# Optimization experiments

Hardware: AMD Instinct MI355X
Metric: run time of the kernel (lower is better)

## Reference

```python
import jax, jax.numpy as jnp
import numpy as np
from functools import partial


def conv2d(x, w, b, pad):
    # x: [B,C,H,W], w: [O,I,kh,kw]
    out = jax.lax.conv_general_dilated(
        x, w, window_strides=(1, 1), padding=[(pad, pad), (pad, pad)],
        dimension_numbers=("NCHW", "OIHW", "NCHW"))
    return out + b[None, :, None, None]


def maxpool3x3_s1(x):
    return jax.lax.reduce_window(
        x, -jnp.inf, jax.lax.max, (1, 1, 3, 3), (1, 1, 1, 1),
        padding=((0, 0), (0, 0), (1, 1), (1, 1)))


def bilinear_sample(img, y, x):
    # img: [B,C,H,W]; y, x: [B,H,W] float sample coords. Zero outside bounds.
    def one(im, yy, xx):  # im [C,H,W]
        H, W = im.shape[1], im.shape[2]
        y0 = jnp.floor(yy)
        x0 = jnp.floor(xx)
        wy = yy - y0
        wx = xx - x0
        y0i = y0.astype(jnp.int32)
        x0i = x0.astype(jnp.int32)

        def g(yi, xi):
            valid = (yi >= 0) & (yi < H) & (xi >= 0) & (xi < W)
            yc = jnp.clip(yi, 0, H - 1)
            xc = jnp.clip(xi, 0, W - 1)
            return im[:, yc, xc] * valid[None].astype(im.dtype)

        return (g(y0i, x0i) * ((1 - wy) * (1 - wx))[None]
                + g(y0i, x0i + 1) * ((1 - wy) * wx)[None]
                + g(y0i + 1, x0i) * (wy * (1 - wx))[None]
                + g(y0i + 1, x0i + 1) * (wy * wx)[None])

    return jax.vmap(one)(img, y, x)


def deform_conv2d(x, offset, weight, bias, k, pad):
    # torchvision-style: offset [B, 2*k*k, H, W], pairs are (dy, dx) in
    # row-major kernel order. stride=1, dilation=1.
    B, C, H, W = x.shape
    off = offset.reshape(B, k * k, 2, H, W)
    hh = jnp.arange(H, dtype=x.dtype)[None, :, None]  # [1,H,1]
    ww = jnp.arange(W, dtype=x.dtype)[None, None, :]  # [1,1,W]
    out = jnp.zeros((B, weight.shape[0], H, W), x.dtype)
    for t in range(k * k):
        i, j = t // k, t % k
        y = hh + (i - pad) + off[:, t, 0]  # [B,H,W]
        xc = ww + (j - pad) + off[:, t, 1]
        s = bilinear_sample(x, y, xc)      # [B,C,H,W]
        out = out + jnp.einsum("bchw,oc->bohw", s, weight[:, :, i, j])
    return out + bias[None, :, None, None]


def _mk(key, shape, scale=0.05):
    return jax.random.normal(key, shape, dtype=jnp.float32) * scale


def setup_inputs() -> dict:
    key = jax.random.key(0)
    ks = jax.random.split(key, 20)
    C = 512
    Cb = C // 4  # 128
    B, H, W = 8, 64, 64
    return {
        "x": jax.random.normal(ks[0], (B, C, H, W), dtype=jnp.float32),
        "w_b1": _mk(ks[1], (Cb, C, 1, 1)), "b_b1": jnp.zeros((Cb,), jnp.float32),
        "w_b21": _mk(ks[2], (Cb, C, 1, 1)), "b_b21": jnp.zeros((Cb,), jnp.float32),
        "w_off2": _mk(ks[3], (18, Cb, 3, 3), 0.01), "b_off2": jnp.zeros((18,), jnp.float32),
        "w_ddc2": _mk(ks[4], (Cb, Cb, 3, 3)), "b_ddc2": jnp.zeros((Cb,), jnp.float32),
        "w_b31": _mk(ks[5], (Cb, C, 1, 1)), "b_b31": jnp.zeros((Cb,), jnp.float32),
        "w_off3": _mk(ks[6], (50, Cb, 5, 5), 0.01), "b_off3": jnp.zeros((50,), jnp.float32),
        "w_ddc3": _mk(ks[7], (Cb, Cb, 5, 5)), "b_ddc3": jnp.zeros((Cb,), jnp.float32),
        "w_b4": _mk(ks[8], (Cb, C, 1, 1)), "b_b4": jnp.zeros((Cb,), jnp.float32),
        "w_cc": _mk(ks[9], (C, Cb * 4, 1, 1)), "b_cc": jnp.zeros((C,), jnp.float32),
    }


def reference(x, w_b1, b_b1, w_b21, b_b21, w_off2, b_off2, w_ddc2, b_ddc2,
              w_b31, b_b31, w_off3, b_off3, w_ddc3, b_ddc3, w_b4, b_b4,
              w_cc, b_cc):
    b1 = conv2d(x, w_b1, b_b1, 0)

    b2i = conv2d(x, w_b21, b_b21, 0)
    off2 = conv2d(b2i, w_off2, b_off2, 1)
    b2 = deform_conv2d(b2i, off2, w_ddc2, b_ddc2, k=3, pad=1)

    b3i = conv2d(x, w_b31, b_b31, 0)
    off3 = conv2d(b3i, w_off3, b_off3, 2)
    b3 = deform_conv2d(b3i, off3, w_ddc3, b_ddc3, k=5, pad=2)

    b4 = conv2d(maxpool3x3_s1(x), w_b4, b_b4, 0)

    cat = jnp.concatenate([b1, b2, b3, b4], axis=1) * x
    fused = conv2d(cat, w_cc, b_cc, 0)
    return x + jax.nn.sigmoid(fused)
```

## Files before the change

### kernel.cpp

```cpp
#include <hip/hip_runtime.h>
#include <math.h>

#define HW 4096
typedef short short8 __attribute__((ext_vector_type(8)));
typedef float floatx4 __attribute__((ext_vector_type(4)));

#define O_XBT   0ull
#define O_PXB   33554432ull
#define O_CATB  67108864ull
#define O_WPB   100663296ull
#define O_W4B   101056512ull
#define O_WCCB  101187584ull
#define O_WD2T  101711872ull
#define O_WD3T  102006784ull
#define O_WO2T  102825984ull
#define O_WO3T  102973440ull
#define O_T2B   33554432ull
#define O_T3B   41943040ull
#define O_OFF2  50331648ull
#define O_OFF3  52690944ull

__device__ __forceinline__ unsigned short f2b(float f) {
    union { float f; unsigned u; } v; v.f = f;
    unsigned r = v.u + 0x7FFFu + ((v.u >> 16) & 1u);
    return (unsigned short)(r >> 16);
}
__device__ __forceinline__ float lou(unsigned u) {
    union { unsigned u; float f; } v; v.u = u << 16; return v.f;
}
__device__ __forceinline__ float hiu(unsigned u) {
    union { unsigned u; float f; } v; v.u = u & 0xFFFF0000u; return v.f;
}
__device__ __forceinline__ unsigned pk2(float lo, float hi) {
    return (unsigned)f2b(lo) | ((unsigned)f2b(hi) << 16);
}

__global__ __launch_bounds__(256) void k_prepw(
        const float* __restrict__ w1, const float* __restrict__ w21,
        const float* __restrict__ w31, const float* __restrict__ w4,
        const float* __restrict__ wcc, const float* __restrict__ wd2,
        const float* __restrict__ wd3, const float* __restrict__ wo2,
        const float* __restrict__ wo3, unsigned short* __restrict__ ws8) {
    unsigned i = blockIdx.x * 256 + threadIdx.x;
    unsigned short* wpb  = ws8 + (O_WPB  >> 1);
    unsigned short* w4b  = ws8 + (O_W4B  >> 1);
    unsigned short* wccb = ws8 + (O_WCCB >> 1);
    unsigned short* wd2t = ws8 + (O_WD2T >> 1);
    unsigned short* wd3t = ws8 + (O_WD3T >> 1);
    unsigned short* wo2t = ws8 + (O_WO2T >> 1);
    unsigned short* wo3t = ws8 + (O_WO3T >> 1);
    if (i < 196608) {
        int o = i >> 9;
        float v = (o < 128) ? w1[i] : (o < 256) ? w21[i - 65536] : w31[i - 131072];
        wpb[i] = f2b(v);
    } else if (i < 262144) {
        unsigned j = i - 196608; w4b[j] = f2b(w4[j]);
    } else if (i < 524288) {
        unsigned j = i - 262144; wccb[j] = f2b(wcc[j]);
    } else if (i < 671744) {
        unsigned j = i - 524288; int t = j >> 14, o = (j >> 7) & 127, c = j & 127;
        wd2t[j] = f2b(wd2[((o * 128 + c) * 9) + t]);
    } else if (i < 1081344) {
        unsigned j = i - 671744; int t = j >> 14, o = (j >> 7) & 127, c = j & 127;
        wd3t[j] = f2b(wd3[((o * 128 + c) * 25) + t]);
    } else if (i < 1155072) {
        unsigned j = i - 1081344; int t = j >> 13, o = (j >> 7) & 63, c = j & 127;
        wo2t[j] = (o < 18) ? f2b(wo2[((o * 128 + c) * 9) + t]) : 0;
    } else if (i < 1359872) {
        unsigned j = i - 1155072; int t = j >> 13, o = (j >> 7) & 63, c = j & 127;
        wo3t[j] = (o < 50) ? f2b(wo3[((o * 128 + c) * 25) + t]) : 0;
    }
}

__global__ __launch_bounds__(256) void k_xpose(const float* __restrict__ X,
                                               unsigned short* __restrict__ xbT) {
    __shared__ unsigned short t[32][33];
    const int p0 = blockIdx.x * 32, c0 = blockIdx.y * 32, b = blockIdx.z;
    const int tid = threadIdx.x;
    #pragma unroll
    for (int s = 0; s < 4; ++s) {
        int cl = s * 8 + (tid >> 5), pl = tid & 31;
        t[cl][pl] = f2b(X[((size_t)b * 512 + c0 + cl) * HW + p0 + pl]);
    }
    __syncthreads();
    #pragma unroll
    for (int s = 0; s < 4; ++s) {
        int pl = s * 8 + (tid >> 5), cl = tid & 31;
        xbT[((size_t)b * HW + p0 + pl) * 512 + c0 + cl] = t[cl][pl];
    }
}

__global__ __launch_bounds__(256) void k_pool(const unsigned short* __restrict__ xbT,
                                              unsigned short* __restrict__ pxb) {
    unsigned gid = blockIdx.x * 256 + threadIdx.x;
    int b = gid >> 18;
    unsigned rem = gid & 262143;
    int pos = rem >> 6;
    int cg = (rem & 63) * 8;
    int h = pos >> 6, w = pos & 63;
    const unsigned short* img = xbT + (size_t)b * HW * 512;
    float m[8] = {-INFINITY, -INFINITY, -INFINITY, -INFINITY,
                  -INFINITY, -INFINITY, -INFINITY, -INFINITY};
    #pragma unroll
    for (int dy = -1; dy <= 1; ++dy) {
        int hh = h + dy;
        if (hh < 0 || hh >= 64) continue;
        #pragma unroll
        for (int dx = -1; dx <= 1; ++dx) {
            int ww = w + dx;
            if (ww < 0 || ww >= 64) continue;
            uint4 v = *(const uint4*)(img + ((size_t)(hh * 64 + ww)) * 512 + cg);
            unsigned uu[4] = {v.x, v.y, v.z, v.w};
            #pragma unroll
            for (int e = 0; e < 4; ++e) {
                m[2 * e]     = fmaxf(m[2 * e],     lou(uu[e]));
                m[2 * e + 1] = fmaxf(m[2 * e + 1], hiu(uu[e]));
            }
        }
    }
    uint4 o;
    o.x = pk2(m[0], m[1]); o.y = pk2(m[2], m[3]);
    o.z = pk2(m[4], m[5]); o.w = pk2(m[6], m[7]);
    *(uint4*)(pxb + ((size_t)b * HW + pos) * 512 + cg) = o;
}

#define SA(r,c) SM[(r)*40 + (c)]
#define SB(r,c) SM[5120 + (r)*40 + (c)]
#define SC(r,c) SM[(r)*136 + (c)]
__global__ __launch_bounds__(256) void k_gemm(
        const unsigned short* __restrict__ A, const float* __restrict__ bias,
        const unsigned short* __restrict__ Bm,
        unsigned short* __restrict__ dst, int dStride, int dOff) {
    __shared__ unsigned short SM[17408];
    const int tid = threadIdx.x;
    const int n0 = blockIdx.x * 128;
    const int b = blockIdx.z;
    const int wave = tid >> 6, lane = tid & 63, quad = lane >> 4, lr = lane & 15;
    const int m0w = (wave & 1) * 64, n0w = (wave >> 1) * 64;
    const int srow = tid >> 1, skh = (tid & 1) * 16;
    floatx4 acc[4][4] = {};

    for (int k0 = 0; k0 < 512; k0 += 32) {
        const unsigned short* ga = A + (size_t)srow * 512 + k0 + skh;
        uint4 a0 = *(const uint4*)(ga);
        uint4 a1 = *(const uint4*)(ga + 8);
        const unsigned short* gb = Bm + ((size_t)b * HW + n0 + srow) * 512 + k0 + skh;
        uint4 b0 = *(const uint4*)(gb);
        uint4 b1 = *(const uint4*)(gb + 8);
        __syncthreads();
        *(uint4*)&SA(srow, skh) = a0;
        *(uint4*)&SA(srow, skh + 8) = a1;
        *(uint4*)&SB(srow, skh) = b0;
        *(uint4*)&SB(srow, skh + 8) = b1;
        __syncthreads();
        short8 af[4], bf[4];
        #pragma unroll
        for (int i = 0; i < 4; ++i) af[i] = *(short8*)&SA(m0w + i * 16 + lr, quad * 8);
        #pragma unroll
        for (int j = 0; j < 4; ++j) bf[j] = *(short8*)&SB(n0w + j * 16 + lr, quad * 8);
        #pragma unroll
        for (int i = 0; i < 4; ++i)
            #pragma unroll
            for (int j = 0; j < 4; ++j)
                acc[i][j] = __builtin_amdgcn_mfma_f32_16x16x32_bf16(af[i], bf[j], acc[i][j], 0, 0, 0);
    }
    __syncthreads();
    #pragma unroll
    for (int i = 0; i < 4; ++i) {
        float4 bs = *(const float4*)&bias[m0w + i * 16 + quad * 4];
        #pragma unroll
        for (int j = 0; j < 4; ++j) {
            floatx4 v = acc[i][j];
            int pos = n0w + j * 16 + lr;
            int ch = m0w + i * 16 + quad * 4;
            uint2 st;
            st.x = pk2(v[0] + bs.x, v[1] + bs.y);
            st.y = pk2(v[2] + bs.z, v[3] + bs.w);
            *(uint2*)&SC(pos, ch) = st;
        }
    }
    __syncthreads();
    #pragma unroll
    for (int r = 0; r < 8; ++r) {
        int pos = (tid >> 4) + r * 16;
        *(uint4*)&dst[((size_t)b * HW + n0 + pos) * dStride + dOff + (tid & 15) * 8] =
            *(uint4*)&SC(pos, (tid & 15) * 8);
    }
}

template<int KS, int OCH>
__global__ __launch_bounds__(256) void k_offconv(
        const unsigned short* __restrict__ img,
        const unsigned short* __restrict__ woT,
        const float* __restrict__ bias, float* __restrict__ Out) {
    constexpr int PAD = KS / 2;
    constexpr int TT = KS * KS;
    __shared__ unsigned short sW[64][136];
    __shared__ unsigned short sS[64][136];
    const int tid = threadIdx.x;
    const int hrow = blockIdx.x, b = blockIdx.z;
    const int wave = tid >> 6, lane = tid & 63, quad = lane >> 4, lr = lane & 15;
    const int m0w = (wave & 1) * 32, n0w = (wave >> 1) * 32;
    const int row = tid >> 2, q4 = (tid & 3) * 32;
    const unsigned short* ib = img + (size_t)b * HW * 128;
    floatx4 acc[2][2] = {};

    for (int t = 0; t < TT; ++t) {
        int ky = t / KS, kx = t % KS;
        int r = hrow + ky - PAD;
        const uint4* wsrc = (const uint4*)(woT + ((size_t)t * 64 + row) * 128 + q4);
        uint4 wv[4] = {wsrc[0], wsrc[1], wsrc[2], wsrc[3]};
        int xcol = row + kx - PAD;
        uint4 sv[4] = {};
        if ((unsigned)r < 64u && (unsigned)xcol < 64u) {
            const uint4* ssrc = (const uint4*)(ib + ((size_t)(r * 64 + xcol)) * 128 + q4);
            sv[0] = ssrc[0]; sv[1] = ssrc[1]; sv[2] = ssrc[2]; sv[3] = ssrc[3];
        }
        __syncthreads();
        #pragma unroll
        for (int j = 0; j < 4; ++j) {
            *(uint4*)&sW[row][q4 + j * 8] = wv[j];
            *(uint4*)&sS[row][q4 + j * 8] = sv[j];
        }
        __syncthreads();
        #pragma unroll
        for (int ks = 0; ks < 4; ++ks) {
            short8 af[2], bf[2];
            #pragma unroll
            for (int i = 0; i < 2; ++i)
                af[i] = *(short8*)&sW[m0w + i * 16 + lr][ks * 32 + quad * 8];
            #pragma unroll
            for (int j = 0; j < 2; ++j)
                bf[j] = *(short8*)&sS[n0w + j * 16 + lr][ks * 32 + quad * 8];
            #pragma unroll
            for (int i = 0; i < 2; ++i)
                #pragma unroll
                for (int j = 0; j < 2; ++j)
                    acc[i][j] = __builtin_amdgcn_mfma_f32_16x16x32_bf16(af[i], bf[j], acc[i][j], 0, 0, 0);
        }
    }
    #pragma unroll
    for (int i = 0; i < 2; ++i) {
        #pragma unroll
        for (int j = 0; j < 2; ++j) {
            floatx4 v = acc[i][j];
            int col = n0w + j * 16 + lr;
            #pragma unroll
            for (int rg = 0; rg < 4; ++rg) {
                int o = m0w + i * 16 + quad * 4 + rg;
                if (o < OCH)
                    Out[((size_t)b * OCH + o) * HW + hrow * 64 + col] = v[rg] + bias[o];
            }
        }
    }
}

template<int KS>
__global__ __launch_bounds__(512) void k_deform4(
        const unsigned short* __restrict__ img,
        const float* __restrict__ Off,
        const unsigned short* __restrict__ wdT,
        const float* __restrict__ bias,
        unsigned short* __restrict__ catb, int dOff) {
    constexpr int PAD = KS / 2;
    constexpr int TT = KS * KS;
    __shared__ unsigned short sW[128][136];
    __shared__ unsigned short sS[128][136];
    const int tid = threadIdx.x;
    const int hrow0 = blockIdx.x * 2, b = blockIdx.z;
    const int wave = tid >> 6, lane = tid & 63, quad = lane >> 4, lr = lane & 15;
    const int m0w = (wave & 1) * 64, n0w = (wave >> 1) * 32;
    const int pos = tid >> 2, cq = (tid & 3) * 32;
    const int pglob = blockIdx.x * 128 + pos;
    const int h = hrow0 + (pos >> 6), w = pos & 63;
    const unsigned short* ib = img + (size_t)b * HW * 128;
    const float* offb = Off + (size_t)b * 2 * TT * HW;
    floatx4 acc[4][2] = {};

    for (int t = 0; t < TT; ++t) {
        float dy = offb[(size_t)(2 * t) * HW + pglob];
        float dx = offb[(size_t)(2 * t + 1) * HW + pglob];
        float fy = (float)(h + t / KS - PAD) + dy;
        float fx = (float)(w + t % KS - PAD) + dx;
        float y0f = floorf(fy), x0f = floorf(fx);
        float wy = fy - y0f, wx = fx - x0f;
        int y0 = (int)y0f, x0 = (int)x0f;
        float w00 = (1.f - wy) * (1.f - wx), w01 = (1.f - wy) * wx;
        float w10 = wy * (1.f - wx), w11 = wy * wx;
        const uint4* wsrc = (const uint4*)(wdT + ((size_t)t * 128 + (tid >> 2)) * 128 + cq);
        uint4 wv[4] = {wsrc[0], wsrc[1], wsrc[2], wsrc[3]};
        bool yv0 = (unsigned)y0 < 64u, yv1 = (unsigned)(y0 + 1) < 64u;
        bool xv0 = (unsigned)x0 < 64u, xv1 = (unsigned)(x0 + 1) < 64u;
        uint4 cA[4] = {}, cB[4] = {}, cC[4] = {}, cD[4] = {};
        long bidx = (long)(y0 * 64 + x0) * 128 + cq;
        if (yv0 && xv0) { const uint4* p = (const uint4*)(ib + bidx);
            cA[0]=p[0]; cA[1]=p[1]; cA[2]=p[2]; cA[3]=p[3]; }
        if (yv0 && xv1) { const uint4* p = (const uint4*)(ib + bidx + 128);
            cB[0]=p[0]; cB[1]=p[1]; cB[2]=p[2]; cB[3]=p[3]; }
        if (yv1 && xv0) { const uint4* p = (const uint4*)(ib + bidx + 64 * 128);
            cC[0]=p[0]; cC[1]=p[1]; cC[2]=p[2]; cC[3]=p[3]; }
        if (yv1 && xv1) { const uint4* p = (const uint4*)(ib + bidx + 65 * 128);
            cD[0]=p[0]; cD[1]=p[1]; cD[2]=p[2]; cD[3]=p[3]; }
        uint4 outv[4];
        #pragma unroll
        for (int j = 0; j < 4; ++j) {
            unsigned a[4] = {cA[j].x, cA[j].y, cA[j].z, cA[j].w};
            unsigned bb[4] = {cB[j].x, cB[j].y, cB[j].z, cB[j].w};
            unsigned c[4] = {cC[j].x, cC[j].y, cC[j].z, cC[j].w};
            unsigned d[4] = {cD[j].x, cD[j].y, cD[j].z, cD[j].w};
            unsigned r[4];
            #pragma unroll
            for (int e = 0; e < 4; ++e) {
                float lo = w00 * lou(a[e]) + w01 * lou(bb[e]) + w10 * lou(c[e]) + w11 * lou(d[e]);
                float hi = w00 * hiu(a[e]) + w01 * hiu(bb[e]) + w10 * hiu(c[e]) + w11 * hiu(d[e]);
                r[e] = pk2(lo, hi);
            }
            outv[j].x = r[0]; outv[j].y = r[1]; outv[j].z = r[2]; outv[j].w = r[3];
        }
        __syncthreads();
        #pragma unroll
        for (int j = 0; j < 4; ++j) {
            *(uint4*)&sW[tid >> 2][cq + j * 8] = wv[j];
            *(uint4*)&sS[pos][cq + j * 8] = outv[j];
        }
        __syncthreads();
        #pragma unroll
        for (int ks = 0; ks < 4; ++ks) {
            short8 af[4], bf[2];
            #pragma unroll
            for (int i = 0; i < 4; ++i)
                af[i] = *(short8*)&sW[m0w + i * 16 + lr][ks * 32 + quad * 8];
            #pragma unroll
            for (int j = 0; j < 2; ++j)
                bf[j] = *(short8*)&sS[n0w + j * 16 + lr][ks * 32 + quad * 8];
            #pragma unroll
            for (int i = 0; i < 4; ++i)
                #pragma unroll
                for (int j = 0; j < 2; ++j)
                    acc[i][j] = __builtin_amdgcn_mfma_f32_16x16x32_bf16(af[i], bf[j], acc[i][j], 0, 0, 0);
        }
    }
    __syncthreads();
    #pragma unroll
    for (int i = 0; i < 4; ++i) {
        float4 bs = *(const float4*)&bias[m0w + i * 16 + quad * 4];
        #pragma unroll
        for (int j = 0; j < 2; ++j) {
            floatx4 v = acc[i][j];
            int p = n0w + j * 16 + lr;
            int ch = m0w + i * 16 + quad * 4;
            uint2 st;
            st.x = pk2(v[0] + bs.x, v[1] + bs.y);
            st.y = pk2(v[2] + bs.z, v[3] + bs.w);
            *(uint2*)&sW[p][ch] = st;
        }
    }
    __syncthreads();
    #pragma unroll
    for (int r = 0; r < 4; ++r) {
        int p = (tid >> 4) + r * 32;
        *(uint4*)&catb[((size_t)b * HW + blockIdx.x * 128 + p) * 512 + dOff + (tid & 15) * 8] =
            *(uint4*)&sW[p][(tid & 15) * 8];
    }
}

__global__ __launch_bounds__(256) void k_gemm_final(
        const unsigned short* __restrict__ A, const float* __restrict__ bias,
        const unsigned short* __restrict__ catb, const unsigned short* __restrict__ xbT,
        const float* __restrict__ X, float* __restrict__ OutF) {
    __shared__ unsigned short sA[128][40];
    __shared__ unsigned short sB[128][40];
    const int tid = threadIdx.x;
    const int n0 = blockIdx.x * 128;
    const int o0 = blockIdx.y * 128;
    const int b = blockIdx.z;
    const int wave = tid >> 6, lane = tid & 63, quad = lane >> 4, lr = lane & 15;
    const int m0w = (wave & 1) * 64, n0w = (wave >> 1) * 64;
    const int srow = tid >> 1, skh = (tid & 1) * 16;
    floatx4 acc[4][4] = {};

    for (int k0 = 0; k0 < 512; k0 += 32) {
        const unsigned short* ga = A + (size_t)(o0 + srow) * 512 + k0 + skh;
        uint4 a0 = *(const uint4*)(ga);
        uint4 a1 = *(const uint4*)(ga + 8);
        size_t bi = ((size_t)b * HW + n0 + srow) * 512 + k0 + skh;
        uint4 c0 = *(const uint4*)(catb + bi);
        uint4 c1 = *(const uint4*)(catb + bi + 8);
        uint4 x0 = *(const uint4*)(xbT + bi);
        uint4 x1 = *(const uint4*)(xbT + bi + 8);
        unsigned cu[8] = {c0.x, c0.y, c0.z, c0.w, c1.x, c1.y, c1.z, c1.w};
        unsigned xu[8] = {x0.x, x0.y, x0.z, x0.w, x1.x, x1.y, x1.z, x1.w};
        unsigned mu[8];
        #pragma unroll
        for (int e = 0; e < 8; ++e)
            mu[e] = pk2(lou(cu[e]) * lou(xu[e]), hiu(cu[e]) * hiu(xu[e]));
        __syncthreads();
        *(uint4*)&sA[srow][skh] = a0;
        *(uint4*)&sA[srow][skh + 8] = a1;
        uint4 m0v; m0v.x = mu[0]; m0v.y = mu[1]; m0v.z = mu[2]; m0v.w = mu[3];
        uint4 m1v; m1v.x = mu[4]; m1v.y = mu[5]; m1v.z = mu[6]; m1v.w = mu[7];
        *(uint4*)&sB[srow][skh] = m0v;
        *(uint4*)&sB[srow][skh + 8] = m1v;
        __syncthreads();
        short8 af[4], bf[4];
        #pragma unroll
        for (int i = 0; i < 4; ++i) af[i] = *(short8*)&sA[m0w + i * 16 + lr][quad * 8];
        #pragma unroll
        for (int j = 0; j < 4; ++j) bf[j] = *(short8*)&sB[n0w + j * 16 + lr][quad * 8];
        #pragma unroll
        for (int i = 0; i < 4; ++i)
            #pragma unroll
            for (int j = 0; j < 4; ++j)
                acc[i][j] = __builtin_amdgcn_mfma_f32_16x16x32_bf16(af[i], bf[j], acc[i][j], 0, 0, 0);
    }
    #pragma unroll
    for (int i = 0; i < 4; ++i) {
        float4 bs = *(const float4*)&bias[o0 + m0w + i * 16 + quad * 4];
        float bsa[4] = {bs.x, bs.y, bs.z, bs.w};
        #pragma unroll
        for (int j = 0; j < 4; ++j) {
            floatx4 v = acc[i][j];
            int pos = n0 + n0w + j * 16 + lr;
            #pragma unroll
            for (int rg = 0; rg < 4; ++rg) {
                int o = o0 + m0w + i * 16 + quad * 4 + rg;
                float f = v[rg] + bsa[rg];
                float sg = 1.f / (1.f + __expf(-f));
                size_t idx = ((size_t)b * 512 + o) * HW + pos;
                OutF[idx] = X[idx] + sg;
            }
        }
    }
}

extern "C" void kernel_launch(void* const* d_in, const int* in_sizes, int n_in,
                              void* d_out, int out_size, void* d_ws, size_t ws_size,
                              hipStream_t stream) {
    const float* x      = (const float*)d_in[0];
    const float* w_b1   = (const float*)d_in[1];
    const float* b_b1   = (const float*)d_in[2];
    const float* w_b21  = (const float*)d_in[3];
    const float* b_b21  = (const float*)d_in[4];
    const float* w_off2 = (const float*)d_in[5];
    const float* b_off2 = (const float*)d_in[6];
    const float* w_ddc2 = (const float*)d_in[7];
    const float* b_ddc2 = (const float*)d_in[8];
    const float* w_b31  = (const float*)d_in[9];
    const float* b_b31  = (const float*)d_in[10];
    const float* w_off3 = (const float*)d_in[11];
    const float* b_off3 = (const float*)d_in[12];
    const float* w_ddc3 = (const float*)d_in[13];
    const float* b_ddc3 = (const float*)d_in[14];
    const float* w_b4   = (const float*)d_in[15];
    const float* b_b4   = (const float*)d_in[16];
    const float* w_cc   = (const float*)d_in[17];
    const float* b_cc   = (const float*)d_in[18];

    char* wsb = (char*)d_ws;
    unsigned short* ws8  = (unsigned short*)d_ws;
    unsigned short* xbT  = (unsigned short*)(wsb + O_XBT);
    unsigned short* pxb  = (unsigned short*)(wsb + O_PXB);
    unsigned short* catb = (unsigned short*)(wsb + O_CATB);
    unsigned short* wpb  = (unsigned short*)(wsb + O_WPB);
    unsigned short* w4b  = (unsigned short*)(wsb + O_W4B);
    unsigned short* wccb = (unsigned short*)(wsb + O_WCCB);
    unsigned short* wd2t = (unsigned short*)(wsb + O_WD2T);
    unsigned short* wd3t = (unsigned short*)(wsb + O_WD3T);
    unsigned short* wo2t = (unsigned short*)(wsb + O_WO2T);
    unsigned short* wo3t = (unsigned short*)(wsb + O_WO3T);
    unsigned short* t2b  = (unsigned short*)(wsb + O_T2B);
    unsigned short* t3b  = (unsigned short*)(wsb + O_T3B);
    float* off2 = (float*)(wsb + O_OFF2);
    float* off3 = (float*)(wsb + O_OFF3);
    float* out  = (float*)d_out;

    k_prepw<<<dim3(5312), dim3(256), 0, stream>>>(
        w_b1, w_b21, w_b31, w_b4, w_cc, w_ddc2, w_ddc3, w_off2, w_off3, ws8);
    k_xpose<<<dim3(128, 16, 8), dim3(256), 0, stream>>>(x, xbT);
    k_pool<<<dim3(8192), dim3(256), 0, stream>>>(xbT, pxb);
    k_gemm<<<dim3(32, 1, 8), dim3(256), 0, stream>>>(w4b, b_b4, pxb, catb, 512, 384);
    k_gemm<<<dim3(32, 1, 8), dim3(256), 0, stream>>>(wpb, b_b1, xbT, catb, 512, 0);
    k_gemm<<<dim3(32, 1, 8), dim3(256), 0, stream>>>(wpb + 128 * 512, b_b21, xbT, t2b, 128, 0);
    k_gemm<<<dim3(32, 1, 8), dim3(256), 0, stream>>>(wpb + 256 * 512, b_b31, xbT, t3b, 128, 0);
    k_offconv<3, 18><<<dim3(64, 1, 8), dim3(256), 0, stream>>>(t2b, wo2t, b_off2, off2);
    k_offconv<5, 50><<<dim3(64, 1, 8), dim3(256), 0, stream>>>(t3b, wo3t, b_off3, off3);
    k_deform4<3><<<dim3(32, 1, 8), dim3(512), 0, stream>>>(t2b, off2, wd2t, b_ddc2, catb, 128);
    k_deform4<5><<<dim3(32, 1, 8), dim3(512), 0, stream>>>(t3b, off3, wd3t, b_ddc3, catb, 256);
    k_gemm_final<<<dim3(32, 4, 8), dim3(256), 0, stream>>>(wccb, b_cc, catb, xbT, x, out);
}
```

Baseline: 657.4 us.

## Restructure offset conv to reuse a shared input slab across all taps

The offset-conv kernel now handles two output rows per block with 512 threads. It stages a padded input slab (rows plus halo) in shared memory once per 32-channel chunk and loops over all kernel taps against that slab, instead of reloading a shifted input row and the weights from global memory for every tap with two barriers each time. Weights are read straight from global memory as MFMA fragments. Results go through a shared float tile so the output is written with coalesced float4 stores. This cuts redundant global loads and barrier count, at the cost of more shared memory (lower occupancy) and uncached direct weight reads.

```diff
diff --git a/kernel.cpp b/kernel.cpp
--- a/kernel.cpp
+++ b/kernel.cpp
@@ -189,49 +189,58 @@
 }
 
 template<int KS, int OCH>
-__global__ __launch_bounds__(256) void k_offconv(
+__global__ __launch_bounds__(512) void k_offconv2(
         const unsigned short* __restrict__ img,
         const unsigned short* __restrict__ woT,
         const float* __restrict__ bias, float* __restrict__ Out) {
     constexpr int PAD = KS / 2;
     constexpr int TT = KS * KS;
-    __shared__ unsigned short sW[64][136];
-    __shared__ unsigned short sS[64][136];
+    constexpr int SR = 2 + 2 * PAD;
+    constexpr int SC2 = 64 + 2 * PAD;
+    constexpr int NE = SR * SC2;
+    __shared__ unsigned short slab[NE * 36];
+    __shared__ float ctile[64 * 132];
     const int tid = threadIdx.x;
-    const int hrow = blockIdx.x, b = blockIdx.z;
+    const int p0 = blockIdx.x * 128, hrow0 = blockIdx.x * 2, b = blockIdx.z;
     const int wave = tid >> 6, lane = tid & 63, quad = lane >> 4, lr = lane & 15;
-    const int m0w = (wave & 1) * 32, n0w = (wave >> 1) * 32;
-    const int row = tid >> 2, q4 = (tid & 3) * 32;
+    const int wm = wave & 1, wn = wave >> 1;
     const unsigned short* ib = img + (size_t)b * HW * 128;
     floatx4 acc[2][2] = {};
 
-    for (int t = 0; t < TT; ++t) {
-        int ky = t / KS, kx = t % KS;
-        int r = hrow + ky - PAD;
-        const uint4* wsrc = (const uint4*)(woT + ((size_t)t * 64 + row) * 128 + q4);
-        uint4 wv[4] = {wsrc[0], wsrc[1], wsrc[2], wsrc[3]};
-        int xcol = row + kx - PAD;
-        uint4 sv[4] = {};
-        if ((unsigned)r < 64u && (unsigned)xcol < 64u) {
-            const uint4* ssrc = (const uint4*)(ib + ((size_t)(r * 64 + xcol)) * 128 + q4);
-            sv[0] = ssrc[0]; sv[1] = ssrc[1]; sv[2] = ssrc[2]; sv[3] = ssrc[3];
-        }
-        __syncthreads();
-        #pragma unroll
-        for (int j = 0; j < 4; ++j) {
-            *(uint4*)&sW[row][q4 + j * 8] = wv[j];
-            *(uint4*)&sS[row][q4 + j * 8] = sv[j];
-        }
-        __syncthreads();
-        #pragma unroll
-        for (int ks = 0; ks < 4; ++ks) {
+    for (int c0 = 0; c0 < 128; c0 += 32) {
+        __syncthreads();
+        if (tid < NE) {
+            int s = tid / SC2, cl = tid % SC2;
+            int r = hrow0 - PAD + s, cc = cl - PAD;
+            uint4 v0 = {}, v1 = {}, v2 = {}, v3 = {};
+            if ((unsigned)r < 64u && (unsigned)cc < 64u) {
+                const uint4* g = (const uint4*)(ib + ((size_t)(r * 64 + cc)) * 128 + c0);
+                v0 = g[0]; v1 = g[1]; v2 = g[2]; v3 = g[3];
+            }
+            uint2* d2 = (uint2*)&slab[tid * 36];
+            d2[0] = make_uint2(v0.x, v0.y); d2[1] = make_uint2(v0.z, v0.w);
+            d2[2] = make_uint2(v1.x, v1.y); d2[3] = make_uint2(v1.z, v1.w);
+            d2[4] = make_uint2(v2.x, v2.y); d2[5] = make_uint2(v2.z, v2.w);
+            d2[6] = make_uint2(v3.x, v3.y); d2[7] = make_uint2(v3.z, v3.w);
+        }
+        __syncthreads();
+        #pragma unroll
+        for (int t = 0; t < TT; ++t) {
+            const int ky = t / KS, kx = t % KS;
             short8 af[2], bf[2];
             #pragma unroll
             for (int i = 0; i < 2; ++i)
-                af[i] = *(short8*)&sW[m0w + i * 16 + lr][ks * 32 + quad * 8];
-            #pragma unroll
-            for (int j = 0; j < 2; ++j)
-                bf[j] = *(short8*)&sS[n0w + j * 16 + lr][ks * 32 + quad * 8];
+                af[i] = *(const short8*)&woT[((size_t)t * 64 + wm * 32 + i * 16 + lr) * 128
+                                             + c0 + quad * 8];
+            #pragma unroll
+            for (int j = 0; j < 2; ++j) {
+                int p = wn * 32 + j * 16 + lr;
+                int e = ((p >> 6) + ky) * SC2 + (p & 63) + kx;
+                union { uint2 u[2]; short8 s; } bb;
+                const uint2* sp = (const uint2*)&slab[e * 36 + quad * 8];
+                bb.u[0] = sp[0]; bb.u[1] = sp[1];
+                bf[j] = bb.s;
+            }
             #pragma unroll
             for (int i = 0; i < 2; ++i)
                 #pragma unroll
@@ -239,17 +248,30 @@
                     acc[i][j] = __builtin_amdgcn_mfma_f32_16x16x32_bf16(af[i], bf[j], acc[i][j], 0, 0, 0);
         }
     }
-    #pragma unroll
-    for (int i = 0; i < 2; ++i) {
+    __syncthreads();
+    #pragma unroll
+    for (int i = 0; i < 2; ++i)
         #pragma unroll
         for (int j = 0; j < 2; ++j) {
             floatx4 v = acc[i][j];
-            int col = n0w + j * 16 + lr;
-            #pragma unroll
-            for (int rg = 0; rg < 4; ++rg) {
-                int o = m0w + i * 16 + quad * 4 + rg;
-                if (o < OCH)
-                    Out[((size_t)b * OCH + o) * HW + hrow * 64 + col] = v[rg] + bias[o];
+            int p = wn * 32 + j * 16 + lr;
+            int o = wm * 32 + i * 16 + quad * 4;
+            #pragma unroll
+            for (int rg = 0; rg < 4; ++rg)
+                ctile[(o + rg) * 132 + p] = v[rg];
+        }
+    __syncthreads();
+    {
+        int o = tid >> 3, seg = tid & 7;
+        if (o < OCH) {
+            float bs = bias[o];
+            const float* src = &ctile[o * 132 + seg * 16];
+            float* dst = &Out[((size_t)b * OCH + o) * HW + p0 + seg * 16];
+            #pragma unroll
+            for (int q = 0; q < 4; ++q) {
+                float4 v = *(const float4*)(src + q * 4);
+                v.x += bs; v.y += bs; v.z += bs; v.w += bs;
+                *(float4*)(dst + q * 4) = v;
             }
         }
     }
@@ -482,8 +504,8 @@
     k_gemm<<<dim3(32, 1, 8), dim3(256), 0, stream>>>(wpb, b_b1, xbT, catb, 512, 0);
     k_gemm<<<dim3(32, 1, 8), dim3(256), 0, stream>>>(wpb + 128 * 512, b_b21, xbT, t2b, 128, 0);
     k_gemm<<<dim3(32, 1, 8), dim3(256), 0, stream>>>(wpb + 256 * 512, b_b31, xbT, t3b, 128, 0);
-    k_offconv<3, 18><<<dim3(64, 1, 8), dim3(256), 0, stream>>>(t2b, wo2t, b_off2, off2);
-    k_offconv<5, 50><<<dim3(64, 1, 8), dim3(256), 0, stream>>>(t3b, wo3t, b_off3, off3);
+    k_offconv2<3, 18><<<dim3(32, 1, 8), dim3(512), 0, stream>>>(t2b, wo2t, b_off2, off2);
+    k_offconv2<5, 50><<<dim3(32, 1, 8), dim3(512), 0, stream>>>(t3b, wo3t, b_off3, off3);
     k_deform4<3><<<dim3(32, 1, 8), dim3(512), 0, stream>>>(t2b, off2, wd2t, b_ddc2, catb, 128);
     k_deform4<5><<<dim3(32, 1, 8), dim3(512), 0, stream>>>(t3b, off3, wd3t, b_ddc3, catb, 256);
     k_gemm_final<<<dim3(32, 4, 8), dim3(256), 0, stream>>>(wccb, b_cc, catb, xbT, x, out);
```

Result: faster. 550.8 us (-16.2%).
